# Kernel tuning notes

Measured on AMD Instinct MI355X. Metric: run time of the kernel, lower is better.

Reference implementation:

```python
import jax, jax.numpy as jnp
import numpy as np

H, W = 300, 400            # grid_size
RES = 0.1                  # resolution (m/pixel)
X0, X1 = -20.0, 20.0       # x_range
Y0, Y1 = -10.0, 30.0       # y_range
Z0, Z1 = -3.0, 4.0         # z_range
MAX_INT = 255.0            # max_intensity
N_MAX = 128.0              # density_normalize
K_SAMPLES = 512            # >= max Bresenham steps inside grid (diag <= 400)


def _rasterize_polyline(pts_xy):
    """DDA line rasterization of an ego-frame polyline -> [H, W] binary grid.
    Matches the Bresenham + 3x3 stamp (width 2 or 3 -> half_w=1) of the original."""
    px = jnp.trunc((pts_xy[:, 0] - X0) / RES)  # int() truncation as in original
    py = jnp.trunc((pts_xy[:, 1] - Y0) / RES)
    p = jnp.stack([px, py], axis=-1)           # [N, 2] pixel coords (float)
    a, b = p[:-1], p[1:]                        # segment endpoints [S, 2]

    def inb(q):
        return (q[:, 0] >= 0) & (q[:, 0] < W) & (q[:, 1] >= 0) & (q[:, 1] < H)

    valid = inb(a) | inb(b)                     # draw if either endpoint in bounds
    lo = jnp.array([0.0, 0.0], jnp.float32)
    hi = jnp.array([W - 1.0, H - 1.0], jnp.float32)
    a = jnp.clip(a, lo, hi)
    b = jnp.clip(b, lo, hi)

    dmax = jnp.max(jnp.abs(b - a), axis=-1)     # [S] major-axis length in pixels
    k = jnp.arange(K_SAMPLES, dtype=jnp.float32)
    t = jnp.minimum(k[None, :], dmax[:, None]) / jnp.maximum(dmax[:, None], 1.0)
    pts = a[:, None, :] + t[..., None] * (b - a)[:, None, :]   # [S, K, 2]
    pix = jnp.round(pts).astype(jnp.int32)

    offs = jnp.arange(-1, 2)                    # half_w = width//2 = 1 -> 3x3 stamp
    xs = pix[..., 0][..., None, None] + offs[:, None]          # [S, K, 3, 1]
    ys = pix[..., 1][..., None, None] + offs[None, :]          # [S, K, 1, 3]
    xs, ys = jnp.broadcast_arrays(xs, ys)
    val = jnp.broadcast_to(valid.astype(jnp.float32)[:, None, None, None], xs.shape)
    # out-of-bounds stamped pixels are dropped, as in the original bounds check
    return jnp.zeros((H, W), jnp.float32).at[ys, xs].max(val, mode="drop")


def _rasterize_lidar(points):
    """[N,4] (x,y,z,intensity) -> [3,H,W] (height, mean intensity, log density)."""
    x, y, z, inten = points[:, 0], points[:, 1], points[:, 2], points[:, 3]
    mask = (x >= X0) & (x < X1) & (y >= Y0) & (y < Y1)
    px = jnp.clip(((x - X0) / RES).astype(jnp.int32), 0, W - 1)
    py = jnp.clip(((y - Y0) / RES).astype(jnp.int32), 0, H - 1)
    w = mask.astype(jnp.float32)
    neg_inf = jnp.float32(-jnp.inf)

    hmax = jnp.full((H, W), neg_inf, jnp.float32).at[py, px].max(
        jnp.where(mask, z, neg_inf))
    hmax = jnp.where(jnp.isneginf(hmax), 0.0, hmax)  # empty cells -> 0 BEFORE norm

    isum = jnp.zeros((H, W), jnp.float32).at[py, px].add(inten * w)
    cnt = jnp.zeros((H, W), jnp.float32).at[py, px].add(w)
    imean = jnp.where(cnt > 0, isum / jnp.maximum(cnt, 1.0), 0.0)

    h = jnp.clip((hmax - Z0) / (Z1 - Z0), 0.0, 1.0)
    i = jnp.clip(imean / MAX_INT, 0.0, 1.0)
    d = jnp.clip(jnp.log1p(cnt) / jnp.log(1.0 + N_MAX), 0.0, 1.0)
    return jnp.stack([h, i, d])


def setup_inputs() -> dict:
    key = jax.random.key(0)
    k1, k2 = jax.random.split(key)
    # LiDAR: 4M points, slightly wider than the ROI so ~some get filtered
    u = jax.random.uniform(k1, (4_000_000, 4), dtype=jnp.float32)
    lo = jnp.array([-25.0, -15.0, -3.0, 0.0], jnp.float32)
    hi = jnp.array([25.0, 35.0, 4.0, 255.0], jnp.float32)
    lidar_points = lo + u * (hi - lo)
    # trajectory: smooth forward path in ego frame
    ty = jnp.linspace(0.0, 25.0, 50, dtype=jnp.float32)
    tx = 2.0 * jnp.sin(0.3 * ty)
    trajectory = jnp.stack([tx, ty], axis=-1)
    # OSM polyline: random walk in world frame (ego at origin)
    steps = 0.5 * jax.random.normal(k2, (2000, 2), dtype=jnp.float32)
    osm_coords = jnp.cumsum(steps, axis=0) + jnp.array([0.0, 10.0], jnp.float32)
    ego_pose = jnp.zeros((3,), jnp.float32)
    return {"lidar_points": lidar_points, "trajectory": trajectory,
            "osm_coords": osm_coords, "ego_pose": ego_pose}


def reference(lidar_points, trajectory, osm_coords, ego_pose):
    lidar_bev = _rasterize_lidar(lidar_points)                 # [3,H,W]
    traj_bev = _rasterize_polyline(trajectory)[None]           # [1,H,W]
    # world -> ego for OSM coords
    cy, sy = jnp.cos(-ego_pose[2]), jnp.sin(-ego_pose[2])
    d = osm_coords - ego_pose[:2]
    osm_ego = jnp.stack([d[:, 0] * cy - d[:, 1] * sy,
                         d[:, 0] * sy + d[:, 1] * cy], axis=-1)
    map_bev = _rasterize_polyline(osm_ego)[None]               # [1,H,W]
    return jnp.concatenate([lidar_bev, traj_bev, map_bev], axis=0)  # [5,H,W]
```

## Files before the change

### kernel.cpp

```cpp
#include <hip/hip_runtime.h>
#include <math.h>

#define GH 300
#define GW 400
#define GHW (GH * GW)

#define TCOLS 25
#define TROWS 19
#define T_TILES (TCOLS * TROWS)
#define B1 1024
#define Q 16

__device__ __forceinline__ bool bin_point(float x, float y, int& px, int& py) {
    if (!(x >= -20.0f && x < 20.0f && y >= -10.0f && y < 30.0f)) return false;
    float qx = __fmul_rn(__fsub_rn(x, -20.0f), 10.0f);
    float qy = __fmul_rn(__fsub_rn(y, -10.0f), 10.0f);
    px = min(max((int)qx, 0), GW - 1);
    py = min(max((int)qy, 0), GH - 1);
    return true;
}

__device__ __forceinline__ void tile_prefix_wave0(const unsigned* src, unsigned* dst) {
    int lane = threadIdx.x;
    if (lane < 64) {
        unsigned run = 0;
        for (int c = 0; c < T_TILES; c += 64) {
            int idx = c + lane;
            unsigned v = (idx < T_TILES) ? src[idx] : 0u;
            unsigned orig = v;
#pragma unroll
            for (int d = 1; d < 64; d <<= 1) {
                unsigned u = __shfl_up(v, d, 64);
                if (lane >= d) v += u;
            }
            if (idx < T_TILES) dst[idx] = run + (v - orig);
            run += __shfl(v, 63, 64);
        }
        if (lane == 0) dst[T_TILES] = run;
    }
}

__device__ __forceinline__ bool make_record(float4 p, unsigned& rec, int& tile) {
    int px, py;
    if (!bin_point(p.x, p.y, px, py)) return false;
    tile = (py >> 4) * TCOLS + (px >> 4);
    int local = ((py & 15) << 4) | (px & 15);
    int z16 = min(max((int)rintf(__fmul_rn(__fadd_rn(p.z, 3.0f), 65535.0f / 7.0f)), 0), 65535);
    int i8 = min(max((int)rintf(p.w), 0), 255);
    rec = ((unsigned)z16 << 16) | ((unsigned)i8 << 8) | (unsigned)local;
    return true;
}

__global__ __launch_bounds__(256) void p1_kernel(const float4* __restrict__ pts, int n,
                                                 int per_block,
                                                 unsigned* __restrict__ staged,
                                                 unsigned* __restrict__ pref_t,
                                                 float* __restrict__ out) {
    __shared__ unsigned lbuf[256 * Q];
    __shared__ unsigned short ltile[256 * Q];
    __shared__ unsigned cnt[T_TILES];
    __shared__ unsigned pref[T_TILES + 1];
    __shared__ unsigned cur[T_TILES];
    for (int t = threadIdx.x; t < T_TILES; t += 256) cnt[t] = 0;
    float4* z4 = (float4*)(out + 3 * GHW);
    for (int j = blockIdx.x * 256 + (int)threadIdx.x; j < (2 * GHW) / 4; j += B1 * 256)
        z4[j] = make_float4(0.0f, 0.0f, 0.0f, 0.0f);
    __syncthreads();

    int start = blockIdx.x * per_block;
    int end = min(start + per_block, n);
    int nmine = 0;
    int i = start + (int)threadIdx.x;
    for (; i + 7 * 256 < end; i += 8 * 256) {
        float4 p[8];
#pragma unroll
        for (int j = 0; j < 8; ++j) p[j] = pts[i + j * 256];
#pragma unroll
        for (int j = 0; j < 8; ++j) {
            unsigned r;
            int tile;
            if (make_record(p[j], r, tile)) {
                lbuf[nmine * 256 + threadIdx.x] = r;
                ltile[nmine * 256 + threadIdx.x] = (unsigned short)tile;
                ++nmine;
                atomicAdd(&cnt[tile], 1u);
            }
        }
    }
    for (; i < end; i += 256) {
        unsigned r;
        int tile;
        if (make_record(pts[i], r, tile)) {
            lbuf[nmine * 256 + threadIdx.x] = r;
            ltile[nmine * 256 + threadIdx.x] = (unsigned short)tile;
            ++nmine;
            atomicAdd(&cnt[tile], 1u);
        }
    }
    __syncthreads();
    tile_prefix_wave0(cnt, pref);
    __syncthreads();
    for (int t = threadIdx.x; t < T_TILES; t += 256) cur[t] = pref[t];
    for (int t = threadIdx.x; t <= T_TILES; t += 256)
        pref_t[t * B1 + blockIdx.x] = pref[t];
    __syncthreads();
    size_t base = (size_t)blockIdx.x * (size_t)per_block;
    for (int j = 0; j < nmine; ++j) {
        unsigned r = lbuf[j * 256 + threadIdx.x];
        int tile = (int)ltile[j * 256 + threadIdx.x];
        unsigned pos = atomicAdd(&cur[tile], 1u);
        staged[base + pos] = r;
    }
}

__device__ void do_poly_segment(int seg, const float2* __restrict__ traj, int ntraj,
                                const float2* __restrict__ osm, int nosm,
                                const float* __restrict__ ego, float* __restrict__ out) {
    int ntseg = ntraj - 1;
    int noseg = nosm - 1;
    if (seg >= ntseg + noseg) return;
    const float2* pts;
    float* out_ch;
    bool use_ego;
    if (seg < ntseg) {
        pts = traj + seg;
        out_ch = out + 3 * GHW;
        use_ego = false;
    } else {
        pts = osm + (seg - ntseg);
        out_ch = out + 4 * GHW;
        use_ego = true;
    }
    float2 P0 = pts[0];
    float2 P1 = pts[1];
    if (use_ego) {
        float yaw = ego[2];
        float cy = cosf(-yaw), sy = sinf(-yaw);
        float ex = ego[0], ey = ego[1];
        float d0x = __fsub_rn(P0.x, ex), d0y = __fsub_rn(P0.y, ey);
        float d1x = __fsub_rn(P1.x, ex), d1y = __fsub_rn(P1.y, ey);
        P0.x = __fsub_rn(__fmul_rn(d0x, cy), __fmul_rn(d0y, sy));
        P0.y = __fadd_rn(__fmul_rn(d0x, sy), __fmul_rn(d0y, cy));
        P1.x = __fsub_rn(__fmul_rn(d1x, cy), __fmul_rn(d1y, sy));
        P1.y = __fadd_rn(__fmul_rn(d1x, sy), __fmul_rn(d1y, cy));
    }
    double ax = trunc(__ddiv_rn(__dadd_rn((double)P0.x, 20.0), 0.1));
    double ay = trunc(__ddiv_rn(__dadd_rn((double)P0.y, 10.0), 0.1));
    double bx = trunc(__ddiv_rn(__dadd_rn((double)P1.x, 20.0), 0.1));
    double by = trunc(__ddiv_rn(__dadd_rn((double)P1.y, 10.0), 0.1));
    bool inA = (ax >= 0.0) && (ax < (double)GW) && (ay >= 0.0) && (ay < (double)GH);
    bool inB = (bx >= 0.0) && (bx < (double)GW) && (by >= 0.0) && (by < (double)GH);
    if (!(inA || inB)) return;
    ax = fmin(fmax(ax, 0.0), (double)(GW - 1));
    ay = fmin(fmax(ay, 0.0), (double)(GH - 1));
    bx = fmin(fmax(bx, 0.0), (double)(GW - 1));
    by = fmin(fmax(by, 0.0), (double)(GH - 1));
    double dx = __dsub_rn(bx, ax);
    double dy = __dsub_rn(by, ay);
    double dmax = fmax(fabs(dx), fabs(dy));
    double denom = fmax(dmax, 1.0);
    int kmax = (int)dmax;
    for (int k = 0; k <= kmax; ++k) {
        double t = __ddiv_rn(fmin((double)k, dmax), denom);
        double ptx = __dadd_rn(ax, __dmul_rn(t, dx));
        double pty = __dadd_rn(ay, __dmul_rn(t, dy));
        int cx = (int)rint(ptx);
        int cc = (int)rint(pty);
#pragma unroll
        for (int oy = -1; oy <= 1; ++oy) {
#pragma unroll
            for (int ox = -1; ox <= 1; ++ox) {
                int xx = cx + ox;
                int yy = cc + oy;
                if (xx < 0) xx += GW;
                if (yy < 0) yy += GH;
                if (xx >= 0 && xx < GW && yy >= 0 && yy < GH) {
                    out_ch[yy * GW + xx] = 1.0f;
                }
            }
        }
    }
}

__global__ __launch_bounds__(1024) void p2_kernel(const unsigned* __restrict__ staged,
                                                  const unsigned* __restrict__ pref_t,
                                                  int per_block,
                                                  float* __restrict__ out,
                                                  const float2* __restrict__ traj, int ntraj,
                                                  const float2* __restrict__ osm, int nosm,
                                                  const float* __restrict__ ego) {
    if (blockIdx.x >= T_TILES) {
        int seg = (blockIdx.x - T_TILES) * 1024 + (int)threadIdx.x;
        do_poly_segment(seg, traj, ntraj, osm, nosm, ego, out);
        return;
    }
    __shared__ unsigned zmax[256];
    __shared__ unsigned long long ic[256];
    int l = threadIdx.x;
    if (l < 256) {
        zmax[l] = 0;
        ic[l] = 0;
    }
    __syncthreads();

    int bid = blockIdx.x;
    const int NX = 8;
    const int q = T_TILES / NX;
    const int r = T_TILES % NX;
    int xk = bid % NX;
    int jj = bid / NX;
    int t = (xk < r ? xk * (q + 1) : r * (q + 1) + (xk - r) * q) + jj;

    unsigned ks = pref_t[t * B1 + l];
    unsigned ke = pref_t[(t + 1) * B1 + l];
    size_t base = (size_t)l * (size_t)per_block;
    for (unsigned k = ks; k < ke; ++k) {
        unsigned rr = staged[base + k];
        int local = (int)(rr & 255u);
        atomicMax(&zmax[local], rr >> 16);
        atomicAdd(&ic[local], (1ull << 32) | ((rr >> 8) & 255ull));
    }
    __syncthreads();

    if (l < 256) {
        unsigned zfin = zmax[l];
        unsigned long long v = ic[l];
        int trow = t / TCOLS, tcol = t % TCOLS;
        int gy = trow * 16 + (l >> 4);
        int gx = tcol * 16 + (l & 15);
        if (gy < GH) {
            const float inv7 = 1.0f / 7.0f;
            const float invlog129 = 1.0f / 4.8598124043616719e+00f;
            float h, ich, dd;
            if (v == 0) {
                h = fminf(fmaxf(__fmul_rn(3.0f, inv7), 0.0f), 1.0f);
                ich = 0.0f;
                dd = 0.0f;
            } else {
                unsigned cnt = (unsigned)(v >> 32);
                float sum8 = (float)(unsigned)(v & 0xFFFFFFFFull);
                h = fminf((float)zfin * (1.0f / 65535.0f), 1.0f);
                ich = fminf(__fdiv_rn(sum8, __fmul_rn((float)cnt, 255.0f)), 1.0f);
                dd = fminf(__fmul_rn(log1pf((float)cnt), invlog129), 1.0f);
            }
            int idx = gy * GW + gx;
            out[0 * GHW + idx] = h;
            out[1 * GHW + idx] = ich;
            out[2 * GHW + idx] = dd;
        }
    }
}

__global__ __launch_bounds__(256) void polylines_kernel(const float2* __restrict__ traj,
                                                        int ntraj,
                                                        const float2* __restrict__ osm, int nosm,
                                                        const float* __restrict__ ego,
                                                        float* __restrict__ out) {
    int seg = blockIdx.x * 256 + (int)threadIdx.x;
    do_poly_segment(seg, traj, ntraj, osm, nosm, ego, out);
}

__global__ __launch_bounds__(256) void init_kernel(float* __restrict__ out) {
    int i = blockIdx.x * blockDim.x + threadIdx.x;
    if (i < GHW) {
        out[0 * GHW + i] = -INFINITY;
        out[1 * GHW + i] = 0.0f;
        out[2 * GHW + i] = 0.0f;
        out[3 * GHW + i] = 0.0f;
        out[4 * GHW + i] = 0.0f;
    }
}

__device__ __forceinline__ void atomicMaxFloat(float* addr, float val) {
    if (val >= 0.0f) {
        atomicMax((int*)addr, __float_as_int(val));
    } else {
        atomicMin((unsigned int*)addr, (unsigned int)__float_as_int(val));
    }
}

__global__ __launch_bounds__(256) void lidar_kernel(const float4* __restrict__ pts, int n,
                                                    float* __restrict__ out) {
    int i = blockIdx.x * blockDim.x + threadIdx.x;
    if (i >= n) return;
    float4 p = pts[i];
    int px, py;
    if (!bin_point(p.x, p.y, px, py)) return;
    int idx = py * GW + px;
    atomicMaxFloat(&out[0 * GHW + idx], p.z);
    atomicAdd(&out[1 * GHW + idx], p.w);
    atomicAdd(&out[2 * GHW + idx], 1.0f);
}

__global__ __launch_bounds__(256) void finalize_kernel(float* __restrict__ out) {
    int i = blockIdx.x * blockDim.x + threadIdx.x;
    if (i >= GHW) return;
    float hm = out[0 * GHW + i];
    float isum = out[1 * GHW + i];
    float c = out[2 * GHW + i];
    if (hm == -INFINITY) hm = 0.0f;
    const float inv7 = 1.0f / 7.0f;
    const float inv255 = 1.0f / 255.0f;
    const float invlog129 = 1.0f / 4.8598124043616719e+00f;
    float h = fminf(fmaxf(__fmul_rn(__fadd_rn(hm, 3.0f), inv7), 0.0f), 1.0f);
    float im = (c > 0.0f) ? __fdiv_rn(isum, fmaxf(c, 1.0f)) : 0.0f;
    float ich = fminf(fmaxf(__fmul_rn(im, inv255), 0.0f), 1.0f);
    float dd = fminf(fmaxf(__fmul_rn(log1pf(c), invlog129), 0.0f), 1.0f);
    out[0 * GHW + i] = h;
    out[1 * GHW + i] = ich;
    out[2 * GHW + i] = dd;
}

extern "C" void kernel_launch(void* const* d_in, const int* in_sizes, int n_in,
                              void* d_out, int out_size, void* d_ws, size_t ws_size,
                              hipStream_t stream) {
    const float* lidar = (const float*)d_in[0];
    const float* traj = (const float*)d_in[1];
    const float* osm = (const float*)d_in[2];
    const float* ego = (const float*)d_in[3];
    float* out = (float*)d_out;

    int n_lidar = in_sizes[0] / 4;
    int n_traj = in_sizes[1] / 2;
    int n_osm = in_sizes[2] / 2;
    int nseg = (n_traj - 1) + (n_osm - 1);
    int npb = (nseg + 1023) / 1024;

    int per_block = (n_lidar + B1 - 1) / B1;
    size_t staged_bytes = (size_t)B1 * (size_t)per_block * 4;
    size_t pref_bytes = (size_t)(T_TILES + 1) * B1 * 4;
    size_t need = staged_bytes + pref_bytes;

    if (ws_size >= need && per_block <= 256 * Q) {
        char* w = (char*)d_ws;
        unsigned* staged = (unsigned*)w;
        unsigned* pref_t = (unsigned*)(w + staged_bytes);

        p1_kernel<<<B1, 256, 0, stream>>>((const float4*)lidar, n_lidar, per_block, staged,
                                          pref_t, out);
        p2_kernel<<<T_TILES + npb, 1024, 0, stream>>>(staged, pref_t, per_block, out,
                                                      (const float2*)traj, n_traj,
                                                      (const float2*)osm, n_osm, ego);
    } else {
        init_kernel<<<(GHW + 255) / 256, 256, 0, stream>>>(out);
        lidar_kernel<<<(n_lidar + 255) / 256, 256, 0, stream>>>((const float4*)lidar, n_lidar,
                                                                out);
        finalize_kernel<<<(GHW + 255) / 256, 256, 0, stream>>>(out);
        polylines_kernel<<<(nseg + 255) / 256, 256, 0, stream>>>((const float2*)traj, n_traj,
                                                                 (const float2*)osm, n_osm, ego,
                                                                 out);
    }
}
```

Measured before the change: 152.0 us.

## Load-balance tile record consumption via block prefix scan and binary search

Each thread used to walk only its own source bucket's records for the tile, which gives uneven per-thread work when bucket counts vary. The block now computes an exclusive scan of per-bucket counts in shared memory. Records are then distributed evenly across all 1024 threads, and each thread finds its source bucket with a 10-step binary search. This trades load imbalance for the cost of the scan, extra syncs and search per record, and less contiguous global reads.

```diff
diff --git a/kernel.cpp b/kernel.cpp
--- a/kernel.cpp
+++ b/kernel.cpp
@@ -196,12 +196,14 @@
     }
     __shared__ unsigned zmax[256];
     __shared__ unsigned long long ic[256];
+    __shared__ unsigned cumB[B1 + 1];
+    __shared__ unsigned startoff[B1];
+    __shared__ unsigned wsum[16];
     int l = threadIdx.x;
     if (l < 256) {
         zmax[l] = 0;
         ic[l] = 0;
     }
-    __syncthreads();
 
     int bid = blockIdx.x;
     const int NX = 8;
@@ -211,11 +213,45 @@
     int jj = bid / NX;
     int t = (xk < r ? xk * (q + 1) : r * (q + 1) + (xk - r) * q) + jj;
 
-    unsigned ks = pref_t[t * B1 + l];
-    unsigned ke = pref_t[(t + 1) * B1 + l];
-    size_t base = (size_t)l * (size_t)per_block;
-    for (unsigned k = ks; k < ke; ++k) {
-        unsigned rr = staged[base + k];
+    unsigned a0 = pref_t[t * B1 + l];
+    unsigned a1 = pref_t[(t + 1) * B1 + l];
+    unsigned c = a1 - a0;
+    startoff[l] = a0;
+
+    int lane = l & 63, wid = l >> 6;
+    unsigned v = c;
+#pragma unroll
+    for (int d = 1; d < 64; d <<= 1) {
+        unsigned u = __shfl_up(v, d, 64);
+        if (lane >= d) v += u;
+    }
+    if (lane == 63) wsum[wid] = v;
+    __syncthreads();
+    if (l < 16) {
+        unsigned wv = wsum[l];
+        unsigned worig = wv;
+#pragma unroll
+        for (int d = 1; d < 16; d <<= 1) {
+            unsigned u = __shfl_up(wv, d, 16);
+            if (l >= d) wv += u;
+        }
+        wsum[l] = wv - worig;
+    }
+    __syncthreads();
+    unsigned excl = (v - c) + wsum[wid];
+    cumB[l] = excl;
+    if (l == B1 - 1) cumB[B1] = excl + c;
+    __syncthreads();
+
+    unsigned nrec = cumB[B1];
+    for (unsigned k = l; k < nrec; k += 1024) {
+        unsigned lo = 0, hi = B1;
+#pragma unroll
+        for (int it = 0; it < 10; ++it) {
+            unsigned mid = (lo + hi) >> 1;
+            if (cumB[mid] <= k) lo = mid; else hi = mid;
+        }
+        unsigned rr = staged[(size_t)lo * (size_t)per_block + startoff[lo] + (k - cumB[lo])];
         int local = (int)(rr & 255u);
         atomicMax(&zmax[local], rr >> 16);
         atomicAdd(&ic[local], (1ull << 32) | ((rr >> 8) & 255ull));
@@ -224,7 +260,7 @@
 
     if (l < 256) {
         unsigned zfin = zmax[l];
-        unsigned long long v = ic[l];
+        unsigned long long v2 = ic[l];
         int trow = t / TCOLS, tcol = t % TCOLS;
         int gy = trow * 16 + (l >> 4);
         int gx = tcol * 16 + (l & 15);
@@ -232,13 +268,13 @@
             const float inv7 = 1.0f / 7.0f;
             const float invlog129 = 1.0f / 4.8598124043616719e+00f;
             float h, ich, dd;
-            if (v == 0) {
+            if (v2 == 0) {
                 h = fminf(fmaxf(__fmul_rn(3.0f, inv7), 0.0f), 1.0f);
                 ich = 0.0f;
                 dd = 0.0f;
             } else {
-                unsigned cnt = (unsigned)(v >> 32);
-                float sum8 = (float)(unsigned)(v & 0xFFFFFFFFull);
+                unsigned cnt = (unsigned)(v2 >> 32);
+                float sum8 = (float)(unsigned)(v2 & 0xFFFFFFFFull);
                 h = fminf((float)zfin * (1.0f / 65535.0f), 1.0f);
                 ich = fminf(__fdiv_rn(sum8, __fmul_rn((float)cnt, 255.0f)), 1.0f);
                 dd = fminf(__fmul_rn(log1pf((float)cnt), invlog129), 1.0f);
```

Measured after the change: 141.0 us. 1.08x faster.
